# Kernel optimization log

Measured on AMD Instinct MI355X. Metric: run time of the kernel, lower is better.

The kernel has to match this reference:

```python
import jax, jax.numpy as jnp
import numpy as np

B, C3, H, W = 2, 96, 256, 256   # triplane: 3 planes x 32 channels
CP = C3 // 3                    # per-plane channels = MLP in_channels
VV, S = 128 * 128, 32           # rays, steps per ray
HID, OUT = 64, 33               # hidden, out_feature_channels + 1
NEG_SLOPE = 0.01


def leaky(v):
    return jnp.where(v >= 0, v, NEG_SLOPE * v)


def grid_sample(img, grid):
    """Bilinear grid_sample, align_corners=False, zero padding.
    img: (N, C, H, W); grid: (N, Hg, Wg, 2) with (x, y) in [-1, 1].
    Returns (N, C, Hg, Wg)."""
    N, C, Hi, Wi = img.shape
    x = (grid[..., 0] + 1.0) * (Wi * 0.5) - 0.5
    y = (grid[..., 1] + 1.0) * (Hi * 0.5) - 0.5
    x0 = jnp.floor(x)
    y0 = jnp.floor(y)
    wx = x - x0
    wy = y - y0
    imgf = img.reshape(N, C, Hi * Wi)

    def corner(xi, yi, w):
        valid = (xi >= 0) & (xi < Wi) & (yi >= 0) & (yi < Hi)
        xi_c = jnp.clip(xi, 0, Wi - 1).astype(jnp.int32)
        yi_c = jnp.clip(yi, 0, Hi - 1).astype(jnp.int32)
        idx = yi_c * Wi + xi_c                      # (N, Hg, Wg)
        v = jax.vmap(lambda im, ix: im[:, ix])(imgf, idx)  # (N, C, Hg, Wg)
        return v * (w * valid)[:, None, :, :]

    return (corner(x0, y0, (1 - wx) * (1 - wy))
            + corner(x0 + 1, y0, wx * (1 - wy))
            + corner(x0, y0 + 1, (1 - wx) * wy)
            + corner(x0 + 1, y0 + 1, wx * wy))


def setup_inputs() -> dict:
    key = jax.random.key(0)
    ks = jax.random.split(key, 8)
    triplane = jax.random.normal(ks[0], (B, C3, H, W), jnp.float32)
    # points are normalized coordinates in [-1, 1]
    points = jax.random.uniform(ks[1], (B, VV, S, 3), jnp.float32, -1.0, 1.0)
    W0 = jax.random.normal(ks[2], (CP, HID), jnp.float32) * 0.05
    b0 = jnp.zeros((HID,), jnp.float32)
    W1 = jax.random.normal(ks[3], (HID, HID), jnp.float32) * 0.05
    b1 = jnp.zeros((HID,), jnp.float32)
    W2 = jax.random.normal(ks[4], (HID, OUT), jnp.float32) * 0.05
    b2 = jnp.zeros((OUT,), jnp.float32)
    return {"triplane": triplane, "points": points,
            "W0": W0, "b0": b0, "W1": W1, "b1": b1, "W2": W2, "b2": b2}


def reference(triplane, points, W0, b0, W1, b1, W2, b2):
    Bb = triplane.shape[0]
    xy = points[..., 0:2]
    xz = jnp.stack([points[..., 0], points[..., 2]], axis=-1)
    yz = points[..., 1:3]
    # (B, 3, VV, S, 2) -> (B*3, VV, S, 2)
    grid = jnp.stack([xy, xz, yz], axis=1).reshape(Bb * 3, *xy.shape[1:])
    planes = triplane.reshape(Bb * 3, -1, triplane.shape[-2], triplane.shape[-1])
    feat = grid_sample(planes, grid)                      # (B*3, CP, VV, S)
    feat = feat.reshape(Bb, 3, -1, feat.shape[-2], feat.shape[-1]).sum(axis=1)
    feat = feat.transpose(0, 2, 3, 1)                     # (B, VV, S, CP)
    h = leaky(feat @ W0 + b0)
    h = leaky(h @ W1 + b1)
    return h @ W2 + b2                                    # (B, VV, S, OUT)
```

## Files before the change

kernel.cpp:

```cpp
#include <hip/hip_runtime.h>

#define BATCH 2
#define PLANES 3
#define CP 32
#define HH 256
#define WW 256
#define HWSZ 65536
#define HID 64
#define NOUT 33
#define NPTS_TOTAL 1048576
#define PLANE_ELEMS 2097152
#define PLANE_ELEMS_DUP 4194304
#define MPTS 128

typedef unsigned int u32;
typedef unsigned short u16;
typedef float floatx4 __attribute__((ext_vector_type(4)));
typedef short bf16x8 __attribute__((ext_vector_type(8)));

static __device__ __forceinline__ u16 f2bf(float f) {
    u32 u = __float_as_uint(f);
    return (u16)((u + 0x7fffu + ((u >> 16) & 1u)) >> 16);
}
static __device__ __forceinline__ float bflo(u32 u) { return __uint_as_float(u << 16); }
static __device__ __forceinline__ float bfhi(u32 u) { return __uint_as_float(u & 0xffff0000u); }

__global__ __launch_bounds__(256) void transpose_dup_k(const float* __restrict__ tp,
                                                       u16* __restrict__ out) {
    int idx = blockIdx.x * 256 + threadIdx.x;
    int bp = idx >> 16;
    int yx = idx & 65535;
    int x = yx & 255;
    int b = bp / 3, p = bp - 3 * b;
    const float* src = tp + (((size_t)(b * 96 + p * 32)) << 16) + yx;
    const bool hasx1 = (x < 255);
    u16 v0[32], v1[32];
#pragma unroll
    for (int c = 0; c < 32; ++c) {
        v0[c] = f2bf(src[(size_t)c << 16]);
        v1[c] = hasx1 ? f2bf(src[((size_t)c << 16) + 1]) : (u16)0;
    }
    uint4* dst = (uint4*)(out + ((size_t)idx << 6));
#pragma unroll
    for (int i = 0; i < 8; ++i) {
        uint4 w;
        w.x = (u32)v0[4 * i + 0] | ((u32)v1[4 * i + 0] << 16);
        w.y = (u32)v0[4 * i + 1] | ((u32)v1[4 * i + 1] << 16);
        w.z = (u32)v0[4 * i + 2] | ((u32)v1[4 * i + 2] << 16);
        w.w = (u32)v0[4 * i + 3] | ((u32)v1[4 * i + 3] << 16);
        dst[i] = w;
    }
}

__global__ __launch_bounds__(256) void gather_dup_k(const u16* __restrict__ planes,
                                                    const float* __restrict__ points,
                                                    u16* __restrict__ feats) {
    const int task = blockIdx.x * 256 + threadIdx.x;
    const int pt = task >> 3;
    const int o = task & 7;
    const int b = pt >> 19;
    const float px = points[(size_t)pt * 3 + 0];
    const float py = points[(size_t)pt * 3 + 1];
    const float pz = points[(size_t)pt * 3 + 2];

    float acc[4];
#pragma unroll
    for (int j = 0; j < 4; ++j) acc[j] = 0.f;

#pragma unroll
    for (int p = 0; p < PLANES; ++p) {
        const float gx = (p == 2) ? py : px;
        const float gy = (p == 0) ? py : pz;
        const float x = (gx + 1.0f) * 128.0f - 0.5f;
        const float y = (gy + 1.0f) * 128.0f - 0.5f;
        const float xf = floorf(x), yf = floorf(y);
        const float wx = x - xf, wy = y - yf;
        const int ix0 = (int)xf, iy0 = (int)yf;
        const int xb = max(ix0, 0);
        const float ax = (ix0 >= 0) ? (1.f - wx) : wx;
        const float bx = (ix0 >= 0) ? wx : 0.f;
        const u16* pb = planes + ((size_t)(b * 3 + p) << 22);
#pragma unroll
        for (int r = 0; r < 2; ++r) {
            const int iy = iy0 + r;
            const bool vy = (iy >= 0) & (iy < HH);
            const float wrow = (r ? wy : (1.f - wy));
            const float wa = vy ? wrow * ax : 0.f;
            const float wb = vy ? wrow * bx : 0.f;
            const int iyc = min(max(iy, 0), HH - 1);
            const uint4 d = *(const uint4*)(pb + (((size_t)((iyc << 8) | xb)) << 6) + (o << 3));
#pragma unroll
            for (int j = 0; j < 4; ++j) {
                const u32 u = (&d.x)[j];
                acc[j] = fmaf(wa, bflo(u), fmaf(wb, bfhi(u), acc[j]));
            }
        }
    }

    uint2 w;
    w.x = (u32)f2bf(acc[0]) | ((u32)f2bf(acc[1]) << 16);
    w.y = (u32)f2bf(acc[2]) | ((u32)f2bf(acc[3]) << 16);
    *(uint2*)(feats + (size_t)pt * 32 + o * 4) = w;
}

__global__ __launch_bounds__(256) void mlp_k(const u16* __restrict__ feats,
                                             const float* __restrict__ W0,
                                             const float* __restrict__ b0,
                                             const float* __restrict__ W1,
                                             const float* __restrict__ b1,
                                             const float* __restrict__ W2,
                                             const float* __restrict__ b2,
                                             float* __restrict__ out) {
    __shared__ __align__(16) u16 sW0t[64 * 40];
    __shared__ __align__(16) u16 sW1t[64 * 72];
    __shared__ __align__(16) u16 sW2t[48 * 72];
    __shared__ __align__(16) u16 sR0[MPTS * 72];
    __shared__ __align__(16) u16 sR1[MPTS * 72];
    __shared__ float sB0[64], sB1[64], sB2[33];

    const int tid = threadIdx.x;
    for (int i = tid; i < 32 * 64; i += 256) { int k = i >> 6, m = i & 63; sW0t[m * 40 + k] = f2bf(W0[i]); }
    for (int i = tid; i < 64 * 64; i += 256) { int k = i >> 6, m = i & 63; sW1t[m * 72 + k] = f2bf(W1[i]); }
    for (int i = tid; i < 64 * 33; i += 256) { int k = i / 33, m = i - 33 * k; sW2t[m * 72 + k] = f2bf(W2[i]); }
    if (tid < 64) { sB0[tid] = b0[tid]; sB1[tid] = b1[tid]; }
    if (tid < 33) sB2[tid] = b2[tid];

    const size_t pbase = (size_t)blockIdx.x * MPTS;
    for (int i = tid; i < MPTS * 4; i += 256) {
        int pt = i >> 2, q = i & 3;
        uint4 d = *(const uint4*)(feats + (pbase + pt) * 32 + q * 8);
        *(uint4*)(sR0 + pt * 40 + q * 8) = d;
    }
    __syncthreads();

    const int lane = tid & 63, wv = tid >> 6;
    const int ln = lane & 15, qd = lane >> 4;

    bf16x8 a0[4];
#pragma unroll
    for (int mt = 0; mt < 4; ++mt)
        a0[mt] = *(const bf16x8*)(sW0t + (mt * 16 + ln) * 40 + qd * 8);
    bf16x8 bx0[2];
#pragma unroll
    for (int nt = 0; nt < 2; ++nt)
        bx0[nt] = *(const bf16x8*)(sR0 + (wv * 32 + nt * 16 + ln) * 40 + qd * 8);
    floatx4 acc0[2][4];
#pragma unroll
    for (int nt = 0; nt < 2; ++nt)
#pragma unroll
        for (int mt = 0; mt < 4; ++mt) {
            floatx4 z = {0.f, 0.f, 0.f, 0.f};
            acc0[nt][mt] = __builtin_amdgcn_mfma_f32_16x16x32_bf16(a0[mt], bx0[nt], z, 0, 0, 0);
        }
#pragma unroll
    for (int nt = 0; nt < 2; ++nt) {
        const int n = wv * 32 + nt * 16 + ln;
#pragma unroll
        for (int mt = 0; mt < 4; ++mt) {
            u16 p[4];
#pragma unroll
            for (int r = 0; r < 4; ++r) {
                const int m = mt * 16 + qd * 4 + r;
                float v = acc0[nt][mt][r] + sB0[m];
                v = (v >= 0.f) ? v : 0.01f * v;
                p[r] = f2bf(v);
            }
            uint2 dd = make_uint2((u32)p[0] | ((u32)p[1] << 16), (u32)p[2] | ((u32)p[3] << 16));
            *(uint2*)(sR1 + n * 72 + mt * 16 + qd * 4) = dd;
        }
    }

    bf16x8 a1[4][2];
#pragma unroll
    for (int mt = 0; mt < 4; ++mt)
#pragma unroll
        for (int c = 0; c < 2; ++c)
            a1[mt][c] = *(const bf16x8*)(sW1t + (mt * 16 + ln) * 72 + c * 32 + qd * 8);
    floatx4 acc1[2][4];
#pragma unroll
    for (int nt = 0; nt < 2; ++nt) {
        const int n = wv * 32 + nt * 16 + ln;
        bf16x8 bf0 = *(const bf16x8*)(sR1 + n * 72 + qd * 8);
        bf16x8 bf1 = *(const bf16x8*)(sR1 + n * 72 + 32 + qd * 8);
#pragma unroll
        for (int mt = 0; mt < 4; ++mt) {
            floatx4 z = {0.f, 0.f, 0.f, 0.f};
            floatx4 t = __builtin_amdgcn_mfma_f32_16x16x32_bf16(a1[mt][0], bf0, z, 0, 0, 0);
            acc1[nt][mt] = __builtin_amdgcn_mfma_f32_16x16x32_bf16(a1[mt][1], bf1, t, 0, 0, 0);
        }
    }
    __syncthreads();

#pragma unroll
    for (int nt = 0; nt < 2; ++nt) {
        const int n = wv * 32 + nt * 16 + ln;
#pragma unroll
        for (int mt = 0; mt < 4; ++mt) {
            u16 p[4];
#pragma unroll
            for (int r = 0; r < 4; ++r) {
                const int m = mt * 16 + qd * 4 + r;
                float v = acc1[nt][mt][r] + sB1[m];
                v = (v >= 0.f) ? v : 0.01f * v;
                p[r] = f2bf(v);
            }
            uint2 dd = make_uint2((u32)p[0] | ((u32)p[1] << 16), (u32)p[2] | ((u32)p[3] << 16));
            *(uint2*)(sR0 + n * 72 + mt * 16 + qd * 4) = dd;
        }
    }

    bf16x8 a2[3][2];
#pragma unroll
    for (int mt = 0; mt < 3; ++mt)
#pragma unroll
        for (int c = 0; c < 2; ++c)
            a2[mt][c] = *(const bf16x8*)(sW2t + (mt * 16 + ln) * 72 + c * 32 + qd * 8);
    floatx4 acc2[2][3];
#pragma unroll
    for (int nt = 0; nt < 2; ++nt) {
        const int n = wv * 32 + nt * 16 + ln;
        bf16x8 bf0 = *(const bf16x8*)(sR0 + n * 72 + qd * 8);
        bf16x8 bf1 = *(const bf16x8*)(sR0 + n * 72 + 32 + qd * 8);
#pragma unroll
        for (int mt = 0; mt < 3; ++mt) {
            floatx4 z = {0.f, 0.f, 0.f, 0.f};
            floatx4 t = __builtin_amdgcn_mfma_f32_16x16x32_bf16(a2[mt][0], bf0, z, 0, 0, 0);
            acc2[nt][mt] = __builtin_amdgcn_mfma_f32_16x16x32_bf16(a2[mt][1], bf1, t, 0, 0, 0);
        }
    }
    __syncthreads();

    float* sOut = (float*)sR1;
#pragma unroll
    for (int nt = 0; nt < 2; ++nt) {
        const int n = wv * 32 + nt * 16 + ln;
#pragma unroll
        for (int mt = 0; mt < 3; ++mt)
#pragma unroll
            for (int r = 0; r < 4; ++r) {
                const int m = mt * 16 + qd * 4 + r;
                if (m < NOUT) sOut[n * 36 + m] = acc2[nt][mt][r] + sB2[m];
            }
    }
    __syncthreads();

    float* og = out + pbase * NOUT;
    for (int i = tid; i < MPTS * NOUT; i += 256) {
        int n = i / 33, m = i - 33 * n;
        og[i] = sOut[n * 36 + m];
    }
}

__global__ __launch_bounds__(256, 2) void fused_mfma_k(const u16* __restrict__ planes,
                                                       const float* __restrict__ points,
                                                       const float* __restrict__ W0,
                                                       const float* __restrict__ b0,
                                                       const float* __restrict__ W1,
                                                       const float* __restrict__ b1,
                                                       const float* __restrict__ W2,
                                                       const float* __restrict__ b2,
                                                       float* __restrict__ out) {
    __shared__ __align__(16) u16 sW0t[64 * 40];
    __shared__ __align__(16) u16 sW1t[64 * 72];
    __shared__ __align__(16) u16 sW2t[48 * 72];
    __shared__ __align__(16) u16 sR0[MPTS * 72];
    __shared__ __align__(16) u16 sR1[MPTS * 72];
    __shared__ float sB0[64], sB1[64], sB2[33];

    const int tid = threadIdx.x;
    for (int i = tid; i < 32 * 64; i += 256) { int k = i >> 6, m = i & 63; sW0t[m * 40 + k] = f2bf(W0[i]); }
    for (int i = tid; i < 64 * 64; i += 256) { int k = i >> 6, m = i & 63; sW1t[m * 72 + k] = f2bf(W1[i]); }
    for (int i = tid; i < 64 * 33; i += 256) { int k = i / 33, m = i - 33 * k; sW2t[m * 72 + k] = f2bf(W2[i]); }
    if (tid < 64) { sB0[tid] = b0[tid]; sB1[tid] = b1[tid]; }
    if (tid < 33) sB2[tid] = b2[tid];

    const size_t pbase = (size_t)blockIdx.x * MPTS;
    float* sPts = (float*)sR1;
    for (int i = tid; i < MPTS * 3; i += 256) sPts[i] = points[pbase * 3 + i];
    __syncthreads();

    const int bBatch = blockIdx.x >> 12;
#pragma unroll
    for (int t = 0; t < 2; ++t) {
        const int task = t * 256 + tid;
        const int pt = task >> 2, q = task & 3;
        const float px = sPts[pt * 3 + 0];
        const float py = sPts[pt * 3 + 1];
        const float pz = sPts[pt * 3 + 2];
        float acc[8];
#pragma unroll
        for (int j = 0; j < 8; ++j) acc[j] = 0.f;
#pragma unroll
        for (int p = 0; p < PLANES; ++p) {
            const float gx = (p == 2) ? py : px;
            const float gy = (p == 0) ? py : pz;
            const float x = (gx + 1.0f) * 128.0f - 0.5f;
            const float y = (gy + 1.0f) * 128.0f - 0.5f;
            const float xf = floorf(x), yf = floorf(y);
            const float wx = x - xf, wy = y - yf;
            const int ix0 = (int)xf, iy0 = (int)yf;
            const int xb = max(ix0, 0);
            const float ax = (ix0 >= 0) ? (1.f - wx) : wx;
            const float bx = (ix0 >= 0) ? wx : 0.f;
            const u16* pb = planes + ((size_t)(bBatch * 3 + p) << 22);
#pragma unroll
            for (int r = 0; r < 2; ++r) {
                const int iy = iy0 + r;
                const bool vy = (iy >= 0) & (iy < HH);
                const float wrow = (r ? wy : (1.f - wy));
                const float wa = vy ? wrow * ax : 0.f;
                const float wb = vy ? wrow * bx : 0.f;
                const int iyc = min(max(iy, 0), HH - 1);
                const u16* src = pb + (((size_t)((iyc << 8) | xb)) << 6) + (q << 4);
                const uint4 d0 = *(const uint4*)src;
                const uint4 d1 = *(const uint4*)(src + 8);
#pragma unroll
                for (int j = 0; j < 4; ++j) {
                    const u32 u = (&d0.x)[j];
                    acc[j] = fmaf(wa, bflo(u), fmaf(wb, bfhi(u), acc[j]));
                    const u32 u2 = (&d1.x)[j];
                    acc[4 + j] = fmaf(wa, bflo(u2), fmaf(wb, bfhi(u2), acc[4 + j]));
                }
            }
        }
        uint4 o;
        o.x = (u32)f2bf(acc[0]) | ((u32)f2bf(acc[1]) << 16);
        o.y = (u32)f2bf(acc[2]) | ((u32)f2bf(acc[3]) << 16);
        o.z = (u32)f2bf(acc[4]) | ((u32)f2bf(acc[5]) << 16);
        o.w = (u32)f2bf(acc[6]) | ((u32)f2bf(acc[7]) << 16);
        *(uint4*)(sR0 + pt * 40 + q * 8) = o;
    }
    __syncthreads();

    const int lane = tid & 63, wv = tid >> 6;
    const int ln = lane & 15, qd = lane >> 4;

    bf16x8 a0[4];
#pragma unroll
    for (int mt = 0; mt < 4; ++mt)
        a0[mt] = *(const bf16x8*)(sW0t + (mt * 16 + ln) * 40 + qd * 8);
    bf16x8 bx0[2];
#pragma unroll
    for (int nt = 0; nt < 2; ++nt)
        bx0[nt] = *(const bf16x8*)(sR0 + (wv * 32 + nt * 16 + ln) * 40 + qd * 8);
    floatx4 acc0[2][4];
#pragma unroll
    for (int nt = 0; nt < 2; ++nt)
#pragma unroll
        for (int mt = 0; mt < 4; ++mt) {
            floatx4 z = {0.f, 0.f, 0.f, 0.f};
            acc0[nt][mt] = __builtin_amdgcn_mfma_f32_16x16x32_bf16(a0[mt], bx0[nt], z, 0, 0, 0);
        }
#pragma unroll
    for (int nt = 0; nt < 2; ++nt) {
        const int n = wv * 32 + nt * 16 + ln;
#pragma unroll
        for (int mt = 0; mt < 4; ++mt) {
            u16 p[4];
#pragma unroll
            for (int r = 0; r < 4; ++r) {
                const int m = mt * 16 + qd * 4 + r;
                float v = acc0[nt][mt][r] + sB0[m];
                v = (v >= 0.f) ? v : 0.01f * v;
                p[r] = f2bf(v);
            }
            uint2 dd = make_uint2((u32)p[0] | ((u32)p[1] << 16), (u32)p[2] | ((u32)p[3] << 16));
            *(uint2*)(sR1 + n * 72 + mt * 16 + qd * 4) = dd;
        }
    }

    bf16x8 a1[4][2];
#pragma unroll
    for (int mt = 0; mt < 4; ++mt)
#pragma unroll
        for (int c = 0; c < 2; ++c)
            a1[mt][c] = *(const bf16x8*)(sW1t + (mt * 16 + ln) * 72 + c * 32 + qd * 8);
    floatx4 acc1[2][4];
#pragma unroll
    for (int nt = 0; nt < 2; ++nt) {
        const int n = wv * 32 + nt * 16 + ln;
        bf16x8 bf0 = *(const bf16x8*)(sR1 + n * 72 + qd * 8);
        bf16x8 bf1 = *(const bf16x8*)(sR1 + n * 72 + 32 + qd * 8);
#pragma unroll
        for (int mt = 0; mt < 4; ++mt) {
            floatx4 z = {0.f, 0.f, 0.f, 0.f};
            floatx4 t = __builtin_amdgcn_mfma_f32_16x16x32_bf16(a1[mt][0], bf0, z, 0, 0, 0);
            acc1[nt][mt] = __builtin_amdgcn_mfma_f32_16x16x32_bf16(a1[mt][1], bf1, t, 0, 0, 0);
        }
    }
    __syncthreads();

#pragma unroll
    for (int nt = 0; nt < 2; ++nt) {
        const int n = wv * 32 + nt * 16 + ln;
#pragma unroll
        for (int mt = 0; mt < 4; ++mt) {
            u16 p[4];
#pragma unroll
            for (int r = 0; r < 4; ++r) {
                const int m = mt * 16 + qd * 4 + r;
                float v = acc1[nt][mt][r] + sB1[m];
                v = (v >= 0.f) ? v : 0.01f * v;
                p[r] = f2bf(v);
            }
            uint2 dd = make_uint2((u32)p[0] | ((u32)p[1] << 16), (u32)p[2] | ((u32)p[3] << 16));
            *(uint2*)(sR0 + n * 72 + mt * 16 + qd * 4) = dd;
        }
    }

    bf16x8 a2[3][2];
#pragma unroll
    for (int mt = 0; mt < 3; ++mt)
#pragma unroll
        for (int c = 0; c < 2; ++c)
            a2[mt][c] = *(const bf16x8*)(sW2t + (mt * 16 + ln) * 72 + c * 32 + qd * 8);
    floatx4 acc2[2][3];
#pragma unroll
    for (int nt = 0; nt < 2; ++nt) {
        const int n = wv * 32 + nt * 16 + ln;
        bf16x8 bf0 = *(const bf16x8*)(sR0 + n * 72 + qd * 8);
        bf16x8 bf1 = *(const bf16x8*)(sR0 + n * 72 + 32 + qd * 8);
#pragma unroll
        for (int mt = 0; mt < 3; ++mt) {
            floatx4 z = {0.f, 0.f, 0.f, 0.f};
            floatx4 t = __builtin_amdgcn_mfma_f32_16x16x32_bf16(a2[mt][0], bf0, z, 0, 0, 0);
            acc2[nt][mt] = __builtin_amdgcn_mfma_f32_16x16x32_bf16(a2[mt][1], bf1, t, 0, 0, 0);
        }
    }
    __syncthreads();

    float* sOut = (float*)sR1;
#pragma unroll
    for (int nt = 0; nt < 2; ++nt) {
        const int n = wv * 32 + nt * 16 + ln;
#pragma unroll
        for (int mt = 0; mt < 3; ++mt)
#pragma unroll
            for (int r = 0; r < 4; ++r) {
                const int m = mt * 16 + qd * 4 + r;
                if (m < NOUT) sOut[n * 36 + m] = acc2[nt][mt][r] + sB2[m];
            }
    }
    __syncthreads();

    float* og = out + pbase * NOUT;
    for (int i = tid; i < MPTS * NOUT; i += 256) {
        int n = i / 33, m = i - 33 * n;
        og[i] = sOut[n * 36 + m];
    }
}

__global__ __launch_bounds__(256) void fused_fallback_k(const float* __restrict__ planes,
                                                        const float* __restrict__ points,
                                                        const float* __restrict__ W0,
                                                        const float* __restrict__ b0,
                                                        const float* __restrict__ W1,
                                                        const float* __restrict__ b1,
                                                        const float* __restrict__ W2,
                                                        const float* __restrict__ b2,
                                                        float* __restrict__ out) {
    const int tid = threadIdx.x;
    const int pgl = blockIdx.x * 256 + tid;
    const int b = pgl >> 19;
    const float px = points[(size_t)pgl * 3 + 0];
    const float py = points[(size_t)pgl * 3 + 1];
    const float pz = points[(size_t)pgl * 3 + 2];
    float feat[CP];
#pragma unroll
    for (int c = 0; c < CP; ++c) feat[c] = 0.f;
#pragma unroll
    for (int p = 0; p < PLANES; ++p) {
        const float gx = (p == 2) ? py : px;
        const float gy = (p == 0) ? py : pz;
        const float x = (gx + 1.0f) * 128.0f - 0.5f;
        const float y = (gy + 1.0f) * 128.0f - 0.5f;
        const float xf = floorf(x), yf = floorf(y);
        const float wx = x - xf, wy = y - yf;
        const int ix0 = (int)xf, iy0 = (int)yf;
        const float* pb = planes + (((size_t)(b * 96 + p * 32)) << 16);
        auto corner = [&](int ix, int iy, float w) {
            const bool v = (ix >= 0) & (ix < WW) & (iy >= 0) & (iy < HH);
            w = v ? w : 0.f;
            const int ixc = min(max(ix, 0), WW - 1);
            const int iyc = min(max(iy, 0), HH - 1);
            const int yx = (iyc << 8) | ixc;
            const float* src = pb + yx;
#pragma unroll
            for (int c = 0; c < CP; ++c) feat[c] = fmaf(w, src[(size_t)c << 16], feat[c]);
        };
        corner(ix0,     iy0,     (1.f - wx) * (1.f - wy));
        corner(ix0 + 1, iy0,     wx * (1.f - wy));
        corner(ix0,     iy0 + 1, (1.f - wx) * wy);
        corner(ix0 + 1, iy0 + 1, wx * wy);
    }
    float h0[HID];
#pragma unroll
    for (int j = 0; j < HID; ++j) h0[j] = b0[j];
    for (int k = 0; k < CP; ++k) {
        const float f = feat[k];
#pragma unroll
        for (int j = 0; j < HID; ++j) h0[j] = fmaf(f, W0[k * HID + j], h0[j]);
    }
#pragma unroll
    for (int j = 0; j < HID; ++j) h0[j] = (h0[j] >= 0.f) ? h0[j] : 0.01f * h0[j];
    float h1[HID];
#pragma unroll
    for (int j = 0; j < HID; ++j) h1[j] = b1[j];
    for (int k = 0; k < HID; ++k) {
        const float f = h0[k];
#pragma unroll
        for (int j = 0; j < HID; ++j) h1[j] = fmaf(f, W1[k * HID + j], h1[j]);
    }
#pragma unroll
    for (int j = 0; j < HID; ++j) h1[j] = (h1[j] >= 0.f) ? h1[j] : 0.01f * h1[j];
    float o[NOUT];
#pragma unroll
    for (int j = 0; j < NOUT; ++j) o[j] = b2[j];
    for (int k = 0; k < HID; ++k) {
        const float f = h1[k];
#pragma unroll
        for (int j = 0; j < NOUT; ++j) o[j] = fmaf(f, W2[k * NOUT + j], o[j]);
    }
    float* op = out + (size_t)pgl * NOUT;
#pragma unroll
    for (int j = 0; j < NOUT; ++j) op[j] = o[j];
}

extern "C" void kernel_launch(void* const* d_in, const int* in_sizes, int n_in,
                              void* d_out, int out_size, void* d_ws, size_t ws_size,
                              hipStream_t stream) {
    const float* triplane = (const float*)d_in[0];
    const float* points   = (const float*)d_in[1];
    const float* W0 = (const float*)d_in[2];
    const float* b0 = (const float*)d_in[3];
    const float* W1 = (const float*)d_in[4];
    const float* b1 = (const float*)d_in[5];
    const float* W2 = (const float*)d_in[6];
    const float* b2 = (const float*)d_in[7];
    float* out = (float*)d_out;

    const size_t needDup   = (size_t)BATCH * PLANES * PLANE_ELEMS_DUP * sizeof(u16);
    const size_t needFeats = (size_t)NPTS_TOTAL * 32 * sizeof(u16);

    if (d_ws != nullptr && ws_size >= needDup + needFeats) {
        u16* planesW = (u16*)d_ws;
        u16* featsW  = planesW + (size_t)BATCH * PLANES * PLANE_ELEMS_DUP;
        transpose_dup_k<<<(BATCH * PLANES * HWSZ) / 256, 256, 0, stream>>>(triplane, planesW);
        gather_dup_k<<<(NPTS_TOTAL * 8) / 256, 256, 0, stream>>>(planesW, points, featsW);
        mlp_k<<<NPTS_TOTAL / MPTS, 256, 0, stream>>>(featsW, W0, b0, W1, b1, W2, b2, out);
    } else if (d_ws != nullptr && ws_size >= needDup) {
        u16* planesW = (u16*)d_ws;
        transpose_dup_k<<<(BATCH * PLANES * HWSZ) / 256, 256, 0, stream>>>(triplane, planesW);
        fused_mfma_k<<<NPTS_TOTAL / MPTS, 256, 0, stream>>>(planesW, points, W0, b0, W1, b1, W2, b2, out);
    } else {
        fused_fallback_k<<<NPTS_TOTAL / 256, 256, 0, stream>>>(
            triplane, points, W0, b0, W1, b1, W2, b2, out);
    }
}
```

Measured before the change: 417.8 us.

## Fuse triplane gather into MLP kernel and pre-transpose weights to bf16 in global

Replaces the separate gather kernel, which wrote bf16 features to a global buffer, and the MLP kernel with one kernel. Each lane gathers the 16 channels it needs straight into its MFMA B-fragment registers, so the features never make a global round trip. Weights are converted and transposed once by a small prep kernel and read from global/L2 into registers instead of being rebuilt in LDS by every block. Shared memory shrinks to two activation buffers and the kernel asks for 4 blocks per CU. The cost is that gather latency now sits inside the MLP kernel and has to be hidden by occupancy alone.

```diff
diff --git a/kernel.cpp b/kernel.cpp
--- a/kernel.cpp
+++ b/kernel.cpp
@@ -12,6 +12,7 @@
 #define PLANE_ELEMS 2097152
 #define PLANE_ELEMS_DUP 4194304
 #define MPTS 128
+#define GW_ELEMS 9216
 
 typedef unsigned int u32;
 typedef unsigned short u16;
@@ -52,194 +53,210 @@
     }
 }
 
-__global__ __launch_bounds__(256) void gather_dup_k(const u16* __restrict__ planes,
-                                                    const float* __restrict__ points,
-                                                    u16* __restrict__ feats) {
-    const int task = blockIdx.x * 256 + threadIdx.x;
-    const int pt = task >> 3;
-    const int o = task & 7;
-    const int b = pt >> 19;
-    const float px = points[(size_t)pt * 3 + 0];
-    const float py = points[(size_t)pt * 3 + 1];
-    const float pz = points[(size_t)pt * 3 + 2];
-
-    float acc[4];
-#pragma unroll
-    for (int j = 0; j < 4; ++j) acc[j] = 0.f;
-
-#pragma unroll
-    for (int p = 0; p < PLANES; ++p) {
-        const float gx = (p == 2) ? py : px;
-        const float gy = (p == 0) ? py : pz;
-        const float x = (gx + 1.0f) * 128.0f - 0.5f;
-        const float y = (gy + 1.0f) * 128.0f - 0.5f;
-        const float xf = floorf(x), yf = floorf(y);
-        const float wx = x - xf, wy = y - yf;
-        const int ix0 = (int)xf, iy0 = (int)yf;
-        const int xb = max(ix0, 0);
-        const float ax = (ix0 >= 0) ? (1.f - wx) : wx;
-        const float bx = (ix0 >= 0) ? wx : 0.f;
-        const u16* pb = planes + ((size_t)(b * 3 + p) << 22);
-#pragma unroll
-        for (int r = 0; r < 2; ++r) {
-            const int iy = iy0 + r;
-            const bool vy = (iy >= 0) & (iy < HH);
-            const float wrow = (r ? wy : (1.f - wy));
-            const float wa = vy ? wrow * ax : 0.f;
-            const float wb = vy ? wrow * bx : 0.f;
-            const int iyc = min(max(iy, 0), HH - 1);
-            const uint4 d = *(const uint4*)(pb + (((size_t)((iyc << 8) | xb)) << 6) + (o << 3));
-#pragma unroll
-            for (int j = 0; j < 4; ++j) {
-                const u32 u = (&d.x)[j];
-                acc[j] = fmaf(wa, bflo(u), fmaf(wb, bfhi(u), acc[j]));
-            }
-        }
-    }
-
-    uint2 w;
-    w.x = (u32)f2bf(acc[0]) | ((u32)f2bf(acc[1]) << 16);
-    w.y = (u32)f2bf(acc[2]) | ((u32)f2bf(acc[3]) << 16);
-    *(uint2*)(feats + (size_t)pt * 32 + o * 4) = w;
-}
-
-__global__ __launch_bounds__(256) void mlp_k(const u16* __restrict__ feats,
-                                             const float* __restrict__ W0,
-                                             const float* __restrict__ b0,
-                                             const float* __restrict__ W1,
-                                             const float* __restrict__ b1,
-                                             const float* __restrict__ W2,
-                                             const float* __restrict__ b2,
-                                             float* __restrict__ out) {
-    __shared__ __align__(16) u16 sW0t[64 * 40];
-    __shared__ __align__(16) u16 sW1t[64 * 72];
-    __shared__ __align__(16) u16 sW2t[48 * 72];
-    __shared__ __align__(16) u16 sR0[MPTS * 72];
-    __shared__ __align__(16) u16 sR1[MPTS * 72];
-    __shared__ float sB0[64], sB1[64], sB2[33];
+__global__ __launch_bounds__(256) void prep_w_k(const float* __restrict__ W0,
+                                                const float* __restrict__ W1,
+                                                const float* __restrict__ W2,
+                                                u16* __restrict__ gW) {
+    int i = blockIdx.x * 256 + threadIdx.x;
+    if (i < 2048) {
+        int m = i >> 5, k = i & 31;
+        gW[i] = f2bf(W0[k * 64 + m]);
+    } else if (i < 6144) {
+        int j = i - 2048;
+        int m = j >> 6, k = j & 63;
+        gW[i] = f2bf(W1[k * 64 + m]);
+    } else {
+        int j = i - 6144;
+        int m = j >> 6, k = j & 63;
+        gW[i] = (m < NOUT) ? f2bf(W2[k * NOUT + m]) : (u16)0;
+    }
+}
+
+__global__ __launch_bounds__(256, 4) void fused3_k(const u16* __restrict__ planes,
+                                                   const u16* __restrict__ gW,
+                                                   const float* __restrict__ points,
+                                                   const float* __restrict__ b0,
+                                                   const float* __restrict__ b1,
+                                                   const float* __restrict__ b2,
+                                                   float* __restrict__ out) {
+    __shared__ __align__(16) u16 sA[MPTS * 72];
+    __shared__ __align__(16) u16 sB[MPTS * 72];
 
     const int tid = threadIdx.x;
-    for (int i = tid; i < 32 * 64; i += 256) { int k = i >> 6, m = i & 63; sW0t[m * 40 + k] = f2bf(W0[i]); }
-    for (int i = tid; i < 64 * 64; i += 256) { int k = i >> 6, m = i & 63; sW1t[m * 72 + k] = f2bf(W1[i]); }
-    for (int i = tid; i < 64 * 33; i += 256) { int k = i / 33, m = i - 33 * k; sW2t[m * 72 + k] = f2bf(W2[i]); }
-    if (tid < 64) { sB0[tid] = b0[tid]; sB1[tid] = b1[tid]; }
-    if (tid < 33) sB2[tid] = b2[tid];
-
-    const size_t pbase = (size_t)blockIdx.x * MPTS;
-    for (int i = tid; i < MPTS * 4; i += 256) {
-        int pt = i >> 2, q = i & 3;
-        uint4 d = *(const uint4*)(feats + (pbase + pt) * 32 + q * 8);
-        *(uint4*)(sR0 + pt * 40 + q * 8) = d;
-    }
-    __syncthreads();
-
     const int lane = tid & 63, wv = tid >> 6;
     const int ln = lane & 15, qd = lane >> 4;
-
-    bf16x8 a0[4];
-#pragma unroll
-    for (int mt = 0; mt < 4; ++mt)
-        a0[mt] = *(const bf16x8*)(sW0t + (mt * 16 + ln) * 40 + qd * 8);
-    bf16x8 bx0[2];
-#pragma unroll
-    for (int nt = 0; nt < 2; ++nt)
-        bx0[nt] = *(const bf16x8*)(sR0 + (wv * 32 + nt * 16 + ln) * 40 + qd * 8);
+    const size_t pbase = (size_t)blockIdx.x * MPTS;
+    const int bBatch = blockIdx.x >> 12;
+
+    bf16x8 bfr[2];
+#pragma unroll
+    for (int it = 0; it < 2; ++it) {
+        const int pt = wv * 32 + it * 16 + ln;
+        const size_t gpt = pbase + pt;
+        const float px = points[gpt * 3 + 0];
+        const float py = points[gpt * 3 + 1];
+        const float pz = points[gpt * 3 + 2];
+        float acc[8];
+#pragma unroll
+        for (int j = 0; j < 8; ++j) acc[j] = 0.f;
+#pragma unroll
+        for (int p = 0; p < PLANES; ++p) {
+            const float gx = (p == 2) ? py : px;
+            const float gy = (p == 0) ? py : pz;
+            const float x = (gx + 1.0f) * 128.0f - 0.5f;
+            const float y = (gy + 1.0f) * 128.0f - 0.5f;
+            const float xf = floorf(x), yf = floorf(y);
+            const float wx = x - xf, wy = y - yf;
+            const int ix0 = (int)xf, iy0 = (int)yf;
+            const int xb = max(ix0, 0);
+            const float wA0 = (ix0 >= 0) ? (1.f - wx) : wx;
+            const float wB0 = (ix0 >= 0) ? wx : 0.f;
+            const u16* pb = planes + ((size_t)(bBatch * 3 + p) << 22);
+#pragma unroll
+            for (int r = 0; r < 2; ++r) {
+                const int iy = iy0 + r;
+                const bool vy = (iy >= 0) & (iy < HH);
+                const float wrow = (r ? wy : (1.f - wy));
+                const float wa = vy ? wrow * wA0 : 0.f;
+                const float wb = vy ? wrow * wB0 : 0.f;
+                const int iyc = min(max(iy, 0), HH - 1);
+                const u16* src = pb + (((size_t)((iyc << 8) | xb)) << 6) + (qd << 4);
+                const uint4 d0 = *(const uint4*)src;
+                const uint4 d1 = *(const uint4*)(src + 8);
+#pragma unroll
+                for (int j = 0; j < 4; ++j) {
+                    const u32 u = (&d0.x)[j];
+                    acc[j] = fmaf(wa, bflo(u), fmaf(wb, bfhi(u), acc[j]));
+                    const u32 u2 = (&d1.x)[j];
+                    acc[4 + j] = fmaf(wa, bflo(u2), fmaf(wb, bfhi(u2), acc[4 + j]));
+                }
+            }
+        }
+        u32 w[4];
+#pragma unroll
+        for (int j = 0; j < 4; ++j)
+            w[j] = (u32)f2bf(acc[2 * j]) | ((u32)f2bf(acc[2 * j + 1]) << 16);
+        bf16x8 v;
+        ((u32*)&v)[0] = w[0]; ((u32*)&v)[1] = w[1];
+        ((u32*)&v)[2] = w[2]; ((u32*)&v)[3] = w[3];
+        bfr[it] = v;
+    }
+
     floatx4 acc0[2][4];
-#pragma unroll
-    for (int nt = 0; nt < 2; ++nt)
-#pragma unroll
-        for (int mt = 0; mt < 4; ++mt) {
-            floatx4 z = {0.f, 0.f, 0.f, 0.f};
-            acc0[nt][mt] = __builtin_amdgcn_mfma_f32_16x16x32_bf16(a0[mt], bx0[nt], z, 0, 0, 0);
-        }
-#pragma unroll
-    for (int nt = 0; nt < 2; ++nt) {
-        const int n = wv * 32 + nt * 16 + ln;
-#pragma unroll
-        for (int mt = 0; mt < 4; ++mt) {
-            u16 p[4];
+    {
+        bf16x8 a0[4];
+#pragma unroll
+        for (int mt = 0; mt < 4; ++mt)
+            a0[mt] = *(const bf16x8*)(gW + (mt * 16 + ln) * 32 + qd * 8);
+#pragma unroll
+        for (int it = 0; it < 2; ++it)
+#pragma unroll
+            for (int mt = 0; mt < 4; ++mt) {
+                floatx4 z = {0.f, 0.f, 0.f, 0.f};
+                acc0[it][mt] = __builtin_amdgcn_mfma_f32_16x16x32_bf16(a0[mt], bfr[it], z, 0, 0, 0);
+            }
+    }
+    {
+        float4 bias0[4];
+#pragma unroll
+        for (int mt = 0; mt < 4; ++mt) bias0[mt] = *(const float4*)(b0 + mt * 16 + qd * 4);
+#pragma unroll
+        for (int it = 0; it < 2; ++it) {
+            const int n = wv * 32 + it * 16 + ln;
+#pragma unroll
+            for (int mt = 0; mt < 4; ++mt) {
+                u16 p[4];
+#pragma unroll
+                for (int r = 0; r < 4; ++r) {
+                    float v = acc0[it][mt][r] + (&bias0[mt].x)[r];
+                    v = (v >= 0.f) ? v : 0.01f * v;
+                    p[r] = f2bf(v);
+                }
+                uint2 dd = make_uint2((u32)p[0] | ((u32)p[1] << 16), (u32)p[2] | ((u32)p[3] << 16));
+                *(uint2*)(sB + n * 72 + mt * 16 + qd * 4) = dd;
+            }
+        }
+    }
+    __syncthreads();
+
+    floatx4 acc1[2][4];
+    {
+        const u16* gW1 = gW + 2048;
+        bf16x8 a1[4][2];
+#pragma unroll
+        for (int mt = 0; mt < 4; ++mt)
+#pragma unroll
+            for (int c = 0; c < 2; ++c)
+                a1[mt][c] = *(const bf16x8*)(gW1 + (mt * 16 + ln) * 64 + c * 32 + qd * 8);
+#pragma unroll
+        for (int it = 0; it < 2; ++it) {
+            const int n = wv * 32 + it * 16 + ln;
+            bf16x8 f0 = *(const bf16x8*)(sB + n * 72 + qd * 8);
+            bf16x8 f1 = *(const bf16x8*)(sB + n * 72 + 32 + qd * 8);
+#pragma unroll
+            for (int mt = 0; mt < 4; ++mt) {
+                floatx4 z = {0.f, 0.f, 0.f, 0.f};
+                floatx4 t = __builtin_amdgcn_mfma_f32_16x16x32_bf16(a1[mt][0], f0, z, 0, 0, 0);
+                acc1[it][mt] = __builtin_amdgcn_mfma_f32_16x16x32_bf16(a1[mt][1], f1, t, 0, 0, 0);
+            }
+        }
+    }
+    {
+        float4 bias1[4];
+#pragma unroll
+        for (int mt = 0; mt < 4; ++mt) bias1[mt] = *(const float4*)(b1 + mt * 16 + qd * 4);
+#pragma unroll
+        for (int it = 0; it < 2; ++it) {
+            const int n = wv * 32 + it * 16 + ln;
+#pragma unroll
+            for (int mt = 0; mt < 4; ++mt) {
+                u16 p[4];
+#pragma unroll
+                for (int r = 0; r < 4; ++r) {
+                    float v = acc1[it][mt][r] + (&bias1[mt].x)[r];
+                    v = (v >= 0.f) ? v : 0.01f * v;
+                    p[r] = f2bf(v);
+                }
+                uint2 dd = make_uint2((u32)p[0] | ((u32)p[1] << 16), (u32)p[2] | ((u32)p[3] << 16));
+                *(uint2*)(sA + n * 72 + mt * 16 + qd * 4) = dd;
+            }
+        }
+    }
+    __syncthreads();
+
+    floatx4 acc2[2][3];
+    {
+        const u16* gW2 = gW + 6144;
+        bf16x8 a2[3][2];
+#pragma unroll
+        for (int mt = 0; mt < 3; ++mt)
+#pragma unroll
+            for (int c = 0; c < 2; ++c)
+                a2[mt][c] = *(const bf16x8*)(gW2 + (mt * 16 + ln) * 64 + c * 32 + qd * 8);
+#pragma unroll
+        for (int it = 0; it < 2; ++it) {
+            const int n = wv * 32 + it * 16 + ln;
+            bf16x8 f0 = *(const bf16x8*)(sA + n * 72 + qd * 8);
+            bf16x8 f1 = *(const bf16x8*)(sA + n * 72 + 32 + qd * 8);
+#pragma unroll
+            for (int mt = 0; mt < 3; ++mt) {
+                floatx4 z = {0.f, 0.f, 0.f, 0.f};
+                floatx4 t = __builtin_amdgcn_mfma_f32_16x16x32_bf16(a2[mt][0], f0, z, 0, 0, 0);
+                acc2[it][mt] = __builtin_amdgcn_mfma_f32_16x16x32_bf16(a2[mt][1], f1, t, 0, 0, 0);
+            }
+        }
+    }
+
+    float* sOut = (float*)sB;
+#pragma unroll
+    for (int it = 0; it < 2; ++it) {
+        const int n = wv * 32 + it * 16 + ln;
+#pragma unroll
+        for (int mt = 0; mt < 3; ++mt)
 #pragma unroll
             for (int r = 0; r < 4; ++r) {
                 const int m = mt * 16 + qd * 4 + r;
-                float v = acc0[nt][mt][r] + sB0[m];
-                v = (v >= 0.f) ? v : 0.01f * v;
-                p[r] = f2bf(v);
-            }
-            uint2 dd = make_uint2((u32)p[0] | ((u32)p[1] << 16), (u32)p[2] | ((u32)p[3] << 16));
-            *(uint2*)(sR1 + n * 72 + mt * 16 + qd * 4) = dd;
-        }
-    }
-
-    bf16x8 a1[4][2];
-#pragma unroll
-    for (int mt = 0; mt < 4; ++mt)
-#pragma unroll
-        for (int c = 0; c < 2; ++c)
-            a1[mt][c] = *(const bf16x8*)(sW1t + (mt * 16 + ln) * 72 + c * 32 + qd * 8);
-    floatx4 acc1[2][4];
-#pragma unroll
-    for (int nt = 0; nt < 2; ++nt) {
-        const int n = wv * 32 + nt * 16 + ln;
-        bf16x8 bf0 = *(const bf16x8*)(sR1 + n * 72 + qd * 8);
-        bf16x8 bf1 = *(const bf16x8*)(sR1 + n * 72 + 32 + qd * 8);
-#pragma unroll
-        for (int mt = 0; mt < 4; ++mt) {
-            floatx4 z = {0.f, 0.f, 0.f, 0.f};
-            floatx4 t = __builtin_amdgcn_mfma_f32_16x16x32_bf16(a1[mt][0], bf0, z, 0, 0, 0);
-            acc1[nt][mt] = __builtin_amdgcn_mfma_f32_16x16x32_bf16(a1[mt][1], bf1, t, 0, 0, 0);
-        }
-    }
-    __syncthreads();
-
-#pragma unroll
-    for (int nt = 0; nt < 2; ++nt) {
-        const int n = wv * 32 + nt * 16 + ln;
-#pragma unroll
-        for (int mt = 0; mt < 4; ++mt) {
-            u16 p[4];
-#pragma unroll
-            for (int r = 0; r < 4; ++r) {
-                const int m = mt * 16 + qd * 4 + r;
-                float v = acc1[nt][mt][r] + sB1[m];
-                v = (v >= 0.f) ? v : 0.01f * v;
-                p[r] = f2bf(v);
-            }
-            uint2 dd = make_uint2((u32)p[0] | ((u32)p[1] << 16), (u32)p[2] | ((u32)p[3] << 16));
-            *(uint2*)(sR0 + n * 72 + mt * 16 + qd * 4) = dd;
-        }
-    }
-
-    bf16x8 a2[3][2];
-#pragma unroll
-    for (int mt = 0; mt < 3; ++mt)
-#pragma unroll
-        for (int c = 0; c < 2; ++c)
-            a2[mt][c] = *(const bf16x8*)(sW2t + (mt * 16 + ln) * 72 + c * 32 + qd * 8);
-    floatx4 acc2[2][3];
-#pragma unroll
-    for (int nt = 0; nt < 2; ++nt) {
-        const int n = wv * 32 + nt * 16 + ln;
-        bf16x8 bf0 = *(const bf16x8*)(sR0 + n * 72 + qd * 8);
-        bf16x8 bf1 = *(const bf16x8*)(sR0 + n * 72 + 32 + qd * 8);
-#pragma unroll
-        for (int mt = 0; mt < 3; ++mt) {
-            floatx4 z = {0.f, 0.f, 0.f, 0.f};
-            floatx4 t = __builtin_amdgcn_mfma_f32_16x16x32_bf16(a2[mt][0], bf0, z, 0, 0, 0);
-            acc2[nt][mt] = __builtin_amdgcn_mfma_f32_16x16x32_bf16(a2[mt][1], bf1, t, 0, 0, 0);
-        }
-    }
-    __syncthreads();
-
-    float* sOut = (float*)sR1;
-#pragma unroll
-    for (int nt = 0; nt < 2; ++nt) {
-        const int n = wv * 32 + nt * 16 + ln;
-#pragma unroll
-        for (int mt = 0; mt < 3; ++mt)
-#pragma unroll
-            for (int r = 0; r < 4; ++r) {
-                const int m = mt * 16 + qd * 4 + r;
-                if (m < NOUT) sOut[n * 36 + m] = acc2[nt][mt][r] + sB2[m];
+                if (m < NOUT) sOut[n * 36 + m] = acc2[it][mt][r] + b2[m];
             }
     }
     __syncthreads();
@@ -539,15 +556,16 @@
     const float* b2 = (const float*)d_in[7];
     float* out = (float*)d_out;
 
-    const size_t needDup   = (size_t)BATCH * PLANES * PLANE_ELEMS_DUP * sizeof(u16);
-    const size_t needFeats = (size_t)NPTS_TOTAL * 32 * sizeof(u16);
-
-    if (d_ws != nullptr && ws_size >= needDup + needFeats) {
+    const size_t dupElems = (size_t)BATCH * PLANES * PLANE_ELEMS_DUP;
+    const size_t needDup  = dupElems * sizeof(u16);
+    const size_t needAll  = needDup + GW_ELEMS * sizeof(u16);
+
+    if (d_ws != nullptr && ws_size >= needAll) {
         u16* planesW = (u16*)d_ws;
-        u16* featsW  = planesW + (size_t)BATCH * PLANES * PLANE_ELEMS_DUP;
+        u16* gW      = planesW + dupElems;
         transpose_dup_k<<<(BATCH * PLANES * HWSZ) / 256, 256, 0, stream>>>(triplane, planesW);
-        gather_dup_k<<<(NPTS_TOTAL * 8) / 256, 256, 0, stream>>>(planesW, points, featsW);
-        mlp_k<<<NPTS_TOTAL / MPTS, 256, 0, stream>>>(featsW, W0, b0, W1, b1, W2, b2, out);
+        prep_w_k<<<GW_ELEMS / 256, 256, 0, stream>>>(W0, W1, W2, gW);
+        fused3_k<<<NPTS_TOTAL / MPTS, 256, 0, stream>>>(planesW, gW, points, b0, b1, b2, out);
     } else if (d_ws != nullptr && ws_size >= needDup) {
         u16* planesW = (u16*)d_ws;
         transpose_dup_k<<<(BATCH * PLANES * HWSZ) / 256, 256, 0, stream>>>(triplane, planesW);
```

Measured after the change: 370.5 us. 1.13x faster.
